# Kernel tuning notes

Hardware: AMD Instinct MI355X
Metric: run time of the kernel (lower is better)

## Reference

```python
import jax, jax.numpy as jnp
import numpy as np

D_MODEL, D_K, D_V, N_HEADS = 1024, 64, 64, 16
B, S = 4, 2048


def setup_inputs() -> dict:
    key = jax.random.key(0)
    ks = jax.random.split(key, 11)
    sd = 0.02
    return {
        "q": jax.random.normal(ks[0], (B, S, D_MODEL), jnp.float32),
        "k": jax.random.normal(ks[1], (B, S, D_MODEL), jnp.float32),
        "v": jax.random.normal(ks[2], (B, S, D_MODEL), jnp.float32),
        # stacked per-head projection weights (equivalent to n_heads separate nn.Linear)
        "Wq": jax.random.normal(ks[3], (N_HEADS, D_MODEL, D_K), jnp.float32) * sd,
        "bq": jax.random.normal(ks[4], (N_HEADS, D_K), jnp.float32) * sd,
        "Wk": jax.random.normal(ks[5], (N_HEADS, D_MODEL, D_K), jnp.float32) * sd,
        "bk": jax.random.normal(ks[6], (N_HEADS, D_K), jnp.float32) * sd,
        "Wv": jax.random.normal(ks[7], (N_HEADS, D_MODEL, D_V), jnp.float32) * sd,
        "bv": jax.random.normal(ks[8], (N_HEADS, D_V), jnp.float32) * sd,
        "Wo": jax.random.normal(ks[9], (N_HEADS * D_V, D_MODEL), jnp.float32) * sd,
        "bo": jax.random.normal(ks[10], (D_MODEL,), jnp.float32) * sd,
    }


def reference(q, k, v, Wq, bq, Wk, bk, Wv, bv, Wo, bo):
    # Per-head projections, batched over heads: (B,S,D) x (H,D,dk) -> (B,H,S,dk)
    qh = jnp.einsum("bsd,hdk->bhsk", q, Wq) + bq[None, :, None, :]
    kh = jnp.einsum("bsd,hdk->bhsk", k, Wk) + bk[None, :, None, :]
    vh = jnp.einsum("bsd,hdk->bhsk", v, Wv) + bv[None, :, None, :]
    # scaled dot-product attention per head
    scores = jnp.einsum("bhqk,bhsk->bhqs", qh, kh) / jnp.sqrt(jnp.float32(D_K))
    attn = jax.nn.softmax(scores, axis=-1)
    ctx = jnp.einsum("bhqs,bhsv->bhqv", attn, vh)  # (B,H,S,dv)
    # concat heads -> (B,S,H*dv), then output projection
    ctx = jnp.transpose(ctx, (0, 2, 1, 3)).reshape(B, S, N_HEADS * D_V)
    return ctx @ Wo + bo
```

## Files before the change

### kernel.cpp

```cpp
#include <hip/hip_runtime.h>
#include <hip/hip_bf16.h>

#define DM 1024
#define SEQ 2048
#define NB 4
#define NH 16
#define DKV 64

typedef unsigned short u16;
typedef unsigned int u32;
typedef __attribute__((ext_vector_type(8))) short bf16x8;
typedef __attribute__((ext_vector_type(4))) float f32x4;

__device__ __forceinline__ u16 f2bf(float f) {
    union { float f; unsigned u; } x; x.f = f;
    unsigned r = x.u + 0x7fffu + ((x.u >> 16) & 1u);
    return (u16)(r >> 16);
}
__device__ __forceinline__ u16 f2bf1(float f) {
    union { float f; unsigned u; } x; x.f = f;
    return (u16)((x.u + 0x8000u) >> 16);
}
__device__ __forceinline__ u32 pack2bf(float a, float b) {
    union { float f; unsigned u; } xa, xb; xa.f = a; xb.f = b;
    return __builtin_amdgcn_perm(xb.u + 0x8000u, xa.u + 0x8000u, 0x07060302);
}

#define GLDS16(gp, lp) __builtin_amdgcn_global_load_lds( \
    (const __attribute__((address_space(1))) u32*)(const void*)(gp), \
    (__attribute__((address_space(3))) u32*)(void*)(lp), 16, 0, 0)

__global__ __launch_bounds__(256)
void transpose_to_bf16(const float* __restrict__ src, u16* __restrict__ dst,
                       int R, int C, long srcHeadStride, long dstHeadStride) {
    int h = blockIdx.z;
    src += (long)h * srcHeadStride;
    dst += (long)h * dstHeadStride;
    __shared__ float tile[32][33];
    int r0 = blockIdx.y * 32, c0 = blockIdx.x * 32;
    int tc = threadIdx.x & 31, tr = threadIdx.x >> 5;
    for (int j = 0; j < 4; j++) {
        int r = tr + j * 8;
        tile[r][tc] = src[(long)(r0 + r) * C + c0 + tc];
    }
    __syncthreads();
    for (int j = 0; j < 4; j++) {
        int rr = tr + j * 8;
        dst[(long)(c0 + rr) * R + r0 + tc] = f2bf(tile[tc][rr]);
    }
}

__global__ __launch_bounds__(256)
void cvt_f32_bf16(const float* __restrict__ src, u16* __restrict__ dst, int n4) {
    int i = blockIdx.x * 256 + threadIdx.x;
    int stride = gridDim.x * 256;
    for (; i < n4; i += stride) {
        float4 v = ((const float4*)src)[i];
        uint2 o; o.x = pack2bf(v.x, v.y); o.y = pack2bf(v.z, v.w);
        ((uint2*)dst)[i] = o;
    }
}

template<int OUTMODE>
__global__ __launch_bounds__(256)
void gemm_bf16(const u16* __restrict__ A, const u16* __restrict__ Bt,
               const float* __restrict__ bias, void* __restrict__ Cptr, float cscale) {
    const int bm0 = blockIdx.x * 128;
    const int bn0 = blockIdx.y * 128;
    __shared__ __align__(16) u16 AsL[2][128 * 64];
    __shared__ __align__(16) u16 BsL[2][128 * 64];
    const int tid = threadIdx.x;
    const int lane = tid & 63;
    const int wave = tid >> 6;
    const int wm = (wave >> 1) * 64, wn = (wave & 1) * 64;
    const int l15 = lane & 15, quad = lane >> 4;

    f32x4 acc[4][4];
    for (int i = 0; i < 4; i++) for (int j = 0; j < 4; j++) acc[i][j] = (f32x4)0.0f;

    int rr[4], cc[4];
    for (int j = 0; j < 4; j++) {
        int ci = (wave * 4 + j) * 64 + lane;
        rr[j] = ci >> 3;
        cc[j] = (ci & 7) ^ (rr[j] & 7);
    }
    const int swz = l15 & 7;

    for (int j = 0; j < 4; j++)
        GLDS16(A + (size_t)(bm0 + rr[j]) * DM + cc[j] * 8, &AsL[0][(wave * 4 + j) * 512]);
    for (int j = 0; j < 4; j++)
        GLDS16(Bt + (size_t)(bn0 + rr[j]) * DM + cc[j] * 8, &BsL[0][(wave * 4 + j) * 512]);

    int buf = 0;
    for (int kk = 0; kk < DM; kk += 64) {
        __syncthreads();
        if (kk + 64 < DM) {
            for (int j = 0; j < 4; j++)
                GLDS16(A + (size_t)(bm0 + rr[j]) * DM + kk + 64 + cc[j] * 8, &AsL[buf ^ 1][(wave * 4 + j) * 512]);
            for (int j = 0; j < 4; j++)
                GLDS16(Bt + (size_t)(bn0 + rr[j]) * DM + kk + 64 + cc[j] * 8, &BsL[buf ^ 1][(wave * 4 + j) * 512]);
        }
        for (int ks = 0; ks < 2; ks++) {
            bf16x8 a[4], b[4];
            const int fo = ((ks * 4 + quad) ^ swz) * 8;
            for (int mi = 0; mi < 4; mi++)
                a[mi] = *(const bf16x8*)&AsL[buf][(wm + mi * 16 + l15) * 64 + fo];
            for (int ni = 0; ni < 4; ni++)
                b[ni] = *(const bf16x8*)&BsL[buf][(wn + ni * 16 + l15) * 64 + fo];
            for (int mi = 0; mi < 4; mi++)
                for (int ni = 0; ni < 4; ni++)
                    acc[mi][ni] = __builtin_amdgcn_mfma_f32_16x16x32_bf16(a[mi], b[ni], acc[mi][ni], 0, 0, 0);
        }
        buf ^= 1;
    }
    for (int mi = 0; mi < 4; mi++) {
        for (int ni = 0; ni < 4; ni++) {
            int n = bn0 + wn + ni * 16 + l15;
            float bb = bias[n];
            int m0 = bm0 + wm + mi * 16 + quad * 4;
            float v0 = (acc[mi][ni][0] + bb) * cscale, v1 = (acc[mi][ni][1] + bb) * cscale;
            float v2 = (acc[mi][ni][2] + bb) * cscale, v3 = (acc[mi][ni][3] + bb) * cscale;
            if (OUTMODE == 0) {
                float* C = (float*)Cptr;
                C[(size_t)(m0 + 0) * DM + n] = v0;
                C[(size_t)(m0 + 1) * DM + n] = v1;
                C[(size_t)(m0 + 2) * DM + n] = v2;
                C[(size_t)(m0 + 3) * DM + n] = v3;
            } else if (OUTMODE == 1) {
                u16* C = (u16*)Cptr;
                int b = m0 >> 11, s = m0 & 2047;
                int h = n >> 6, d = n & 63;
                size_t base = (((size_t)(b * NH + h)) * SEQ + s) * DKV + d;
                C[base + 0 * DKV] = f2bf1(v0);
                C[base + 1 * DKV] = f2bf1(v1);
                C[base + 2 * DKV] = f2bf1(v2);
                C[base + 3 * DKV] = f2bf1(v3);
            } else {
                u16* C = (u16*)Cptr;
                int b = m0 >> 11, s = m0 & 2047;
                int h = n >> 6, d = n & 63;
                uint2 pk; pk.x = pack2bf(v0, v1); pk.y = pack2bf(v2, v3);
                *(uint2*)&C[(((size_t)(b * NH + h)) * DKV + d) * SEQ + s] = pk;
            }
        }
    }
}

__global__ __launch_bounds__(256)
void attn_kernel(const u16* __restrict__ qh, const u16* __restrict__ kh,
                 const u16* __restrict__ vt, u16* __restrict__ ctx) {
    const int qblk = blockIdx.x;
    const int h = blockIdx.y;
    const int b = blockIdx.z;
    const int tid = threadIdx.x;
    const int lane = tid & 63;
    const int wave = tid >> 6;
    const int l15 = lane & 15, quad = lane >> 4;
    const size_t headoff = ((size_t)(b * NH + h)) * SEQ * DKV;
    const u16* Q = qh + headoff;
    const u16* K = kh + headoff;
    const u16* V = vt + headoff;
    const int q0 = qblk * 128 + wave * 32;

    __shared__ __align__(16) u16 KsL[2][64 * 64];
    __shared__ __align__(16) u16 VtL[2][64 * 64];
    __shared__ __align__(16) u16 Ps[4][32][72];

    bf16x8 aq[2][2];
    for (int ni = 0; ni < 2; ni++)
        for (int ks = 0; ks < 2; ks++)
            aq[ni][ks] = *(const bf16x8*)&Q[(size_t)(q0 + ni * 16 + l15) * DKV + ks * 32 + quad * 8];

    bf16x8 vones;
    for (int j = 0; j < 8; j++) vones[j] = (short)0x3F80;

    f32x4 ot[4][2];
    for (int di = 0; di < 4; di++) for (int ni = 0; ni < 2; ni++) ot[di][ni] = (f32x4)0.0f;
    f32x4 lacc[2];
    lacc[0] = (f32x4)0.0f; lacc[1] = (f32x4)0.0f;

    int rr[2], cc[2];
    for (int j = 0; j < 2; j++) {
        int ci = (wave * 2 + j) * 64 + lane;
        rr[j] = ci >> 3;
        cc[j] = (ci & 7) ^ (rr[j] & 7);
    }
    const int swz = l15 & 7;

    for (int j = 0; j < 2; j++) {
        GLDS16(K + (size_t)rr[j] * DKV + cc[j] * 8, &KsL[0][(wave * 2 + j) * 512]);
        GLDS16(V + (size_t)rr[j] * SEQ + cc[j] * 8, &VtL[0][(wave * 2 + j) * 512]);
    }

    int buf = 0;
    for (int kv0 = 0; kv0 < SEQ; kv0 += 64) {
        __syncthreads();
        if (kv0 + 64 < SEQ) {
            int nx = kv0 + 64;
            for (int j = 0; j < 2; j++) {
                GLDS16(K + (size_t)(nx + rr[j]) * DKV + cc[j] * 8, &KsL[buf ^ 1][(wave * 2 + j) * 512]);
                GLDS16(V + (size_t)rr[j] * SEQ + nx + cc[j] * 8, &VtL[buf ^ 1][(wave * 2 + j) * 512]);
            }
        }

        f32x4 st[4][2];
        for (int mi = 0; mi < 4; mi++) for (int ni = 0; ni < 2; ni++) st[mi][ni] = (f32x4)0.0f;
        for (int ks = 0; ks < 2; ks++) {
            const int fo = ((ks * 4 + quad) ^ swz) * 8;
            bf16x8 bk[4];
            for (int mi = 0; mi < 4; mi++)
                bk[mi] = *(const bf16x8*)&KsL[buf][(mi * 16 + l15) * 64 + fo];
            for (int mi = 0; mi < 4; mi++)
                for (int ni = 0; ni < 2; ni++)
                    st[mi][ni] = __builtin_amdgcn_mfma_f32_16x16x32_bf16(bk[mi], aq[ni][ks], st[mi][ni], 0, 0, 0);
        }

        for (int ni = 0; ni < 2; ni++) {
            for (int mi = 0; mi < 4; mi++) {
                f32x4 p;
                p.x = exp2f(st[mi][ni].x);
                p.y = exp2f(st[mi][ni].y);
                p.z = exp2f(st[mi][ni].z);
                p.w = exp2f(st[mi][ni].w);
                uint2 pk; pk.x = pack2bf(p.x, p.y); pk.y = pack2bf(p.z, p.w);
                *(uint2*)&Ps[wave][ni * 16 + l15][mi * 16 + quad * 4] = pk;
            }
        }
        __threadfence_block();

        for (int ks = 0; ks < 2; ks++) {
            const int fo = ((ks * 4 + quad) ^ swz) * 8;
            bf16x8 av[4], bp[2];
            for (int di = 0; di < 4; di++)
                av[di] = *(const bf16x8*)&VtL[buf][(di * 16 + l15) * 64 + fo];
            for (int ni = 0; ni < 2; ni++)
                bp[ni] = *(const bf16x8*)&Ps[wave][ni * 16 + l15][ks * 32 + quad * 8];
            for (int di = 0; di < 4; di++)
                for (int ni = 0; ni < 2; ni++)
                    ot[di][ni] = __builtin_amdgcn_mfma_f32_16x16x32_bf16(av[di], bp[ni], ot[di][ni], 0, 0, 0);
            for (int ni = 0; ni < 2; ni++)
                lacc[ni] = __builtin_amdgcn_mfma_f32_16x16x32_bf16(vones, bp[ni], lacc[ni], 0, 0, 0);
        }
        buf ^= 1;
    }

    for (int ni = 0; ni < 2; ni++) {
        float inv = 1.0f / lacc[ni][0];
        int srow = q0 + ni * 16 + l15;
        for (int di = 0; di < 4; di++) {
            uint2 pk;
            pk.x = pack2bf(ot[di][ni].x * inv, ot[di][ni].y * inv);
            pk.y = pack2bf(ot[di][ni].z * inv, ot[di][ni].w * inv);
            *(uint2*)&ctx[((size_t)b * SEQ + srow) * DM + h * DKV + di * 16 + quad * 4] = pk;
        }
    }
}

extern "C" void kernel_launch(void* const* d_in, const int* in_sizes, int n_in,
                              void* d_out, int out_size, void* d_ws, size_t ws_size,
                              hipStream_t stream) {
    const float* q  = (const float*)d_in[0];
    const float* k  = (const float*)d_in[1];
    const float* v  = (const float*)d_in[2];
    const float* Wq = (const float*)d_in[3];
    const float* bq = (const float*)d_in[4];
    const float* Wk = (const float*)d_in[5];
    const float* bk = (const float*)d_in[6];
    const float* Wv = (const float*)d_in[7];
    const float* bv = (const float*)d_in[8];
    const float* Wo = (const float*)d_in[9];
    const float* bo = (const float*)d_in[10];
    float* out = (float*)d_out;

    char* ws = (char*)d_ws;
    const size_t MB = 1024 * 1024;
    u16* WqT = (u16*)(ws + 0 * MB);
    u16* WkT = (u16*)(ws + 2 * MB);
    u16* WvT = (u16*)(ws + 4 * MB);
    u16* WoT = (u16*)(ws + 6 * MB);
    u16* qh  = (u16*)(ws + 8 * MB);
    u16* kh  = (u16*)(ws + 24 * MB);
    u16* vh  = (u16*)(ws + 40 * MB);
    u16* ctx = (u16*)(ws + 56 * MB);
    u16* cvt = ctx;

    const int n4 = NB * SEQ * DM / 4;
    const float SC = 0.125f * 1.44269504088896f;

    transpose_to_bf16<<<dim3(2, 32, 16), 256, 0, stream>>>(Wq, WqT, 1024, 64, 1024 * 64, 64 * 1024);
    transpose_to_bf16<<<dim3(2, 32, 16), 256, 0, stream>>>(Wk, WkT, 1024, 64, 1024 * 64, 64 * 1024);
    transpose_to_bf16<<<dim3(2, 32, 16), 256, 0, stream>>>(Wv, WvT, 1024, 64, 1024 * 64, 64 * 1024);
    transpose_to_bf16<<<dim3(32, 32, 1), 256, 0, stream>>>(Wo, WoT, 1024, 1024, 0, 0);

    cvt_f32_bf16<<<dim3(2048), 256, 0, stream>>>(q, cvt, n4);
    gemm_bf16<1><<<dim3(64, 8), 256, 0, stream>>>(cvt, WqT, bq, qh, SC);
    cvt_f32_bf16<<<dim3(2048), 256, 0, stream>>>(k, cvt, n4);
    gemm_bf16<1><<<dim3(64, 8), 256, 0, stream>>>(cvt, WkT, bk, kh, 1.0f);
    cvt_f32_bf16<<<dim3(2048), 256, 0, stream>>>(v, cvt, n4);
    gemm_bf16<2><<<dim3(64, 8), 256, 0, stream>>>(cvt, WvT, bv, vh, 1.0f);

    attn_kernel<<<dim3(16, 16, 4), 256, 0, stream>>>(qh, kh, vh, ctx);

    gemm_bf16<0><<<dim3(64, 8), 256, 0, stream>>>(ctx, WoT, bo, out, 1.0f);
}
```

Before: 382.9 us.

## Double attention query tile per wave and merge QKV weight transposes

Each attention wave now processes 64 query rows instead of 32, so every K/V tile loaded to LDS is reused across twice as many queries and the grid is halved to 512 blocks. Launch bounds request two blocks per SM to keep occupancy despite larger register and LDS footprints. Separately, the three per-head weight transposes are merged into one launch, with a dedicated kernel for Wo. The risk is higher register pressure and fewer blocks, which may reduce latency hiding on the 256-CU device.

Measured after the change: 372.5 us. 2.7% less time.

```diff
diff --git a/kernel.cpp b/kernel.cpp
--- a/kernel.cpp
+++ b/kernel.cpp
@@ -31,22 +31,42 @@
     (__attribute__((address_space(3))) u32*)(void*)(lp), 16, 0, 0)
 
 __global__ __launch_bounds__(256)
-void transpose_to_bf16(const float* __restrict__ src, u16* __restrict__ dst,
-                       int R, int C, long srcHeadStride, long dstHeadStride) {
-    int h = blockIdx.z;
-    src += (long)h * srcHeadStride;
-    dst += (long)h * dstHeadStride;
+void transpose_qkv_w(const float* __restrict__ s0, const float* __restrict__ s1,
+                     const float* __restrict__ s2, u16* __restrict__ d0,
+                     u16* __restrict__ d1, u16* __restrict__ d2) {
+    int z = blockIdx.z;
+    int which = z >> 4, h = z & 15;
+    const float* src = (which == 0) ? s0 : (which == 1) ? s1 : s2;
+    u16* dst = (which == 0) ? d0 : (which == 1) ? d1 : d2;
+    src += (long)h * 1024 * 64;
+    dst += (long)h * 64 * 1024;
     __shared__ float tile[32][33];
     int r0 = blockIdx.y * 32, c0 = blockIdx.x * 32;
     int tc = threadIdx.x & 31, tr = threadIdx.x >> 5;
     for (int j = 0; j < 4; j++) {
         int r = tr + j * 8;
-        tile[r][tc] = src[(long)(r0 + r) * C + c0 + tc];
+        tile[r][tc] = src[(long)(r0 + r) * 64 + c0 + tc];
     }
     __syncthreads();
     for (int j = 0; j < 4; j++) {
         int rr = tr + j * 8;
-        dst[(long)(c0 + rr) * R + r0 + tc] = f2bf(tile[tc][rr]);
+        dst[(long)(c0 + rr) * 1024 + r0 + tc] = f2bf(tile[tc][rr]);
+    }
+}
+
+__global__ __launch_bounds__(256)
+void transpose_wo(const float* __restrict__ src, u16* __restrict__ dst) {
+    __shared__ float tile[32][33];
+    int r0 = blockIdx.y * 32, c0 = blockIdx.x * 32;
+    int tc = threadIdx.x & 31, tr = threadIdx.x >> 5;
+    for (int j = 0; j < 4; j++) {
+        int r = tr + j * 8;
+        tile[r][tc] = src[(long)(r0 + r) * 1024 + c0 + tc];
+    }
+    __syncthreads();
+    for (int j = 0; j < 4; j++) {
+        int rr = tr + j * 8;
+        dst[(long)(c0 + rr) * 1024 + r0 + tc] = f2bf(tile[tc][rr]);
     }
 }
 
@@ -146,7 +166,7 @@
     }
 }
 
-__global__ __launch_bounds__(256)
+__global__ __launch_bounds__(256, 2)
 void attn_kernel(const u16* __restrict__ qh, const u16* __restrict__ kh,
                  const u16* __restrict__ vt, u16* __restrict__ ctx) {
     const int qblk = blockIdx.x;
@@ -160,24 +180,24 @@
     const u16* Q = qh + headoff;
     const u16* K = kh + headoff;
     const u16* V = vt + headoff;
-    const int q0 = qblk * 128 + wave * 32;
+    const int q0 = qblk * 256 + wave * 64;
 
     __shared__ __align__(16) u16 KsL[2][64 * 64];
     __shared__ __align__(16) u16 VtL[2][64 * 64];
-    __shared__ __align__(16) u16 Ps[4][32][72];
-
-    bf16x8 aq[2][2];
-    for (int ni = 0; ni < 2; ni++)
+    __shared__ __align__(16) u16 Ps[4][64][72];
+
+    bf16x8 aq[4][2];
+    for (int ni = 0; ni < 4; ni++)
         for (int ks = 0; ks < 2; ks++)
             aq[ni][ks] = *(const bf16x8*)&Q[(size_t)(q0 + ni * 16 + l15) * DKV + ks * 32 + quad * 8];
 
     bf16x8 vones;
     for (int j = 0; j < 8; j++) vones[j] = (short)0x3F80;
 
-    f32x4 ot[4][2];
-    for (int di = 0; di < 4; di++) for (int ni = 0; ni < 2; ni++) ot[di][ni] = (f32x4)0.0f;
-    f32x4 lacc[2];
-    lacc[0] = (f32x4)0.0f; lacc[1] = (f32x4)0.0f;
+    f32x4 ot[4][4];
+    for (int di = 0; di < 4; di++) for (int ni = 0; ni < 4; ni++) ot[di][ni] = (f32x4)0.0f;
+    f32x4 lacc[4];
+    for (int ni = 0; ni < 4; ni++) lacc[ni] = (f32x4)0.0f;
 
     int rr[2], cc[2];
     for (int j = 0; j < 2; j++) {
@@ -203,19 +223,19 @@
             }
         }
 
-        f32x4 st[4][2];
-        for (int mi = 0; mi < 4; mi++) for (int ni = 0; ni < 2; ni++) st[mi][ni] = (f32x4)0.0f;
+        f32x4 st[4][4];
+        for (int mi = 0; mi < 4; mi++) for (int ni = 0; ni < 4; ni++) st[mi][ni] = (f32x4)0.0f;
         for (int ks = 0; ks < 2; ks++) {
             const int fo = ((ks * 4 + quad) ^ swz) * 8;
             bf16x8 bk[4];
             for (int mi = 0; mi < 4; mi++)
                 bk[mi] = *(const bf16x8*)&KsL[buf][(mi * 16 + l15) * 64 + fo];
             for (int mi = 0; mi < 4; mi++)
-                for (int ni = 0; ni < 2; ni++)
+                for (int ni = 0; ni < 4; ni++)
                     st[mi][ni] = __builtin_amdgcn_mfma_f32_16x16x32_bf16(bk[mi], aq[ni][ks], st[mi][ni], 0, 0, 0);
         }
 
-        for (int ni = 0; ni < 2; ni++) {
+        for (int ni = 0; ni < 4; ni++) {
             for (int mi = 0; mi < 4; mi++) {
                 f32x4 p;
                 p.x = exp2f(st[mi][ni].x);
@@ -230,21 +250,21 @@
 
         for (int ks = 0; ks < 2; ks++) {
             const int fo = ((ks * 4 + quad) ^ swz) * 8;
-            bf16x8 av[4], bp[2];
+            bf16x8 av[4], bp[4];
             for (int di = 0; di < 4; di++)
                 av[di] = *(const bf16x8*)&VtL[buf][(di * 16 + l15) * 64 + fo];
-            for (int ni = 0; ni < 2; ni++)
+            for (int ni = 0; ni < 4; ni++)
                 bp[ni] = *(const bf16x8*)&Ps[wave][ni * 16 + l15][ks * 32 + quad * 8];
             for (int di = 0; di < 4; di++)
-                for (int ni = 0; ni < 2; ni++)
+                for (int ni = 0; ni < 4; ni++)
                     ot[di][ni] = __builtin_amdgcn_mfma_f32_16x16x32_bf16(av[di], bp[ni], ot[di][ni], 0, 0, 0);
-            for (int ni = 0; ni < 2; ni++)
+            for (int ni = 0; ni < 4; ni++)
                 lacc[ni] = __builtin_amdgcn_mfma_f32_16x16x32_bf16(vones, bp[ni], lacc[ni], 0, 0, 0);
         }
         buf ^= 1;
     }
 
-    for (int ni = 0; ni < 2; ni++) {
+    for (int ni = 0; ni < 4; ni++) {
         float inv = 1.0f / lacc[ni][0];
         int srow = q0 + ni * 16 + l15;
         for (int di = 0; di < 4; di++) {
@@ -287,10 +307,8 @@
     const int n4 = NB * SEQ * DM / 4;
     const float SC = 0.125f * 1.44269504088896f;
 
-    transpose_to_bf16<<<dim3(2, 32, 16), 256, 0, stream>>>(Wq, WqT, 1024, 64, 1024 * 64, 64 * 1024);
-    transpose_to_bf16<<<dim3(2, 32, 16), 256, 0, stream>>>(Wk, WkT, 1024, 64, 1024 * 64, 64 * 1024);
-    transpose_to_bf16<<<dim3(2, 32, 16), 256, 0, stream>>>(Wv, WvT, 1024, 64, 1024 * 64, 64 * 1024);
-    transpose_to_bf16<<<dim3(32, 32, 1), 256, 0, stream>>>(Wo, WoT, 1024, 1024, 0, 0);
+    transpose_qkv_w<<<dim3(2, 32, 48), 256, 0, stream>>>(Wq, Wk, Wv, WqT, WkT, WvT);
+    transpose_wo<<<dim3(32, 32), 256, 0, stream>>>(Wo, WoT);
 
     cvt_f32_bf16<<<dim3(2048), 256, 0, stream>>>(q, cvt, n4);
     gemm_bf16<1><<<dim3(64, 8), 256, 0, stream>>>(cvt, WqT, bq, qh, SC);
@@ -299,7 +317,7 @@
     cvt_f32_bf16<<<dim3(2048), 256, 0, stream>>>(v, cvt, n4);
     gemm_bf16<2><<<dim3(64, 8), 256, 0, stream>>>(cvt, WvT, bv, vh, 1.0f);
 
-    attn_kernel<<<dim3(16, 16, 4), 256, 0, stream>>>(qh, kh, vh, ctx);
+    attn_kernel<<<dim3(8, 16, 4), 256, 0, stream>>>(qh, kh, vh, ctx);
 
     gemm_bf16<0><<<dim3(64, 8), 256, 0, stream>>>(ctx, WoT, bo, out, 1.0f);
 }
```
